# Kernel tuning notes

Hardware: AMD Instinct MI355X
Metric: run time of the kernel (lower is better)

The kernel has to match this reference:

```python
import jax, jax.numpy as jnp
import numpy as np

N, D = 8192, 256
NUM_CLASSES = 64


def setup_inputs() -> dict:
    key = jax.random.key(0)
    k1, k2 = jax.random.split(key)
    represent = jax.random.normal(k1, (N, D), dtype=jnp.float32)
    label = jax.random.randint(k2, (N,), 0, NUM_CLASSES, dtype=jnp.int64)
    t = jnp.float32(0.1)  # temperature
    return {"represent": represent, "label": label, "t": t}


def reference(represent, label, t):
    x = represent.astype(jnp.float32)                      # [N, D]
    norms = jnp.sqrt(jnp.sum(x * x, axis=-1))              # [N]
    # pairwise cosine: (x x^T) / (||xi|| ||xj||)
    cos = (x @ x.T) / (norms[:, None] * norms[None, :])    # [N, N]
    pos_mask = label[:, None] == label[None, :]            # [N, N] bool
    e = jnp.exp(cos / t)                                   # [N, N]
    # original computes exp(mask * cos / t): masked-out entries become exp(0) = 1
    pos_pair = jnp.where(pos_mask, e, 1.0).sum(axis=-1)    # [N]
    neg_pair = jnp.where(pos_mask, 1.0, e).sum(axis=-1)    # [N]
    loss = (jnp.log(neg_pair) - jnp.log(pos_pair)).sum() / represent.shape[0]
    return loss
```

## Files before the change

kernel.cpp:

```cpp
#include <hip/hip_runtime.h>
#include <hip/hip_bf16.h>

#define N_ROWS 8192
#define DIM 256
#define NUM_CLASSES 64
#define NBLK 64
#define NTRI (NBLK * (NBLK + 1) / 2)

typedef __bf16 bf16x8 __attribute__((ext_vector_type(8)));
typedef float f32x4 __attribute__((ext_vector_type(4)));

__device__ __forceinline__ unsigned short f2bf(float f) {
  unsigned int u = __float_as_uint(f);
  u += 0x7fffu + ((u >> 16) & 1u);
  return (unsigned short)(u >> 16);
}
__device__ __forceinline__ float bf2f(unsigned short h) {
  return __uint_as_float(((unsigned int)h) << 16);
}

__device__ __forceinline__ void gload_lds16(const unsigned short* g, unsigned short* l) {
  __builtin_amdgcn_global_load_lds(
      (const __attribute__((address_space(1))) unsigned int*)g,
      (__attribute__((address_space(3))) unsigned int*)l, 16, 0, 0);
}

__global__ void __launch_bounds__(256) prep_kernel(
    const float* __restrict__ x, const float* __restrict__ tptr,
    unsigned short* __restrict__ xb, float* __restrict__ sv,
    float* __restrict__ gsum, unsigned int* __restrict__ gcnt) {
  if (blockIdx.x == 0 && threadIdx.x == 0) { *gsum = 0.f; *gcnt = 0u; }
  const int row = blockIdx.x * 4 + (threadIdx.x >> 6);
  const int lane = threadIdx.x & 63;
  const float4 v = *reinterpret_cast<const float4*>(x + (size_t)row * DIM + lane * 4);
  const unsigned short q0 = f2bf(v.x), q1 = f2bf(v.y), q2 = f2bf(v.z), q3 = f2bf(v.w);
  const float f0 = bf2f(q0), f1 = bf2f(q1), f2 = bf2f(q2), f3 = bf2f(q3);
  float ss = f0 * f0 + f1 * f1 + f2 * f2 + f3 * f3;
  ushort4 u4; u4.x = q0; u4.y = q1; u4.z = q2; u4.w = q3;
  *reinterpret_cast<ushort4*>(xb + (size_t)row * DIM + lane * 4) = u4;
  for (int m = 32; m; m >>= 1) ss += __shfl_xor(ss, m, 64);
  if (lane == 0) {
    const float C = 1.4426950408889634f / tptr[0];
    sv[row] = sqrtf(C / ss);
  }
}

__global__ void __launch_bounds__(256, 3) main_kernel(
    const unsigned short* __restrict__ xb, const float* __restrict__ sv,
    const int* __restrict__ lab, float* __restrict__ part) {
  const int q = blockIdx.x;
  int I = (int)((129.0f - sqrtf(16641.0f - 8.0f * (float)q)) * 0.5f);
  while (I * (129 - I) / 2 > q) --I;
  while ((I + 1) * (128 - I) / 2 <= q) ++I;
  const int J = I + (q - I * (129 - I) / 2);

  __shared__ alignas(16) unsigned short Alds[128 * 32];
  __shared__ alignas(16) unsigned short Blds[128 * 32];
  float* red = reinterpret_cast<float*>(Alds);
  float (*colred)[128][2] = reinterpret_cast<float (*)[128][2]>(Blds);

  const int tid = threadIdx.x;
  const int wave = tid >> 6;
  const int lane = tid & 63;
  const int quad = lane >> 4;
  const int lc = lane & 15;
  const int wrow = (wave >> 1) * 64;
  const int wcol = (wave & 1) * 64;
  const int rowBase = I * 128;
  const int colBase = J * 128;

  f32x4 acc[4][4];
  const f32x4 zero4 = {0.f, 0.f, 0.f, 0.f};
  for (int mi = 0; mi < 4; ++mi)
    for (int ni = 0; ni < 4; ++ni) acc[mi][ni] = zero4;

  const int srow = lane >> 2;
  const int sseg = (lane & 3) * 8;

  for (int kb = 0; kb < 8; ++kb) {
    const int k0 = kb * 32;
    const unsigned short* gA =
        xb + (size_t)(rowBase + wave * 32 + srow) * DIM + k0 + sseg;
    gload_lds16(gA, &Alds[(wave * 32) * 32]);
    gload_lds16(gA + 16 * DIM, &Alds[(wave * 32 + 16) * 32]);
    const unsigned short* gB =
        xb + (size_t)(colBase + wave * 32 + srow) * DIM + k0 + sseg;
    gload_lds16(gB, &Blds[(wave * 32) * 32]);
    gload_lds16(gB + 16 * DIM, &Blds[(wave * 32 + 16) * 32]);
    __syncthreads();
    bf16x8 afr[4], bfr[4];
    for (int mi = 0; mi < 4; ++mi)
      afr[mi] = *reinterpret_cast<const bf16x8*>(
          &Alds[(wrow + mi * 16 + lc) * 32 + quad * 8]);
    for (int ni = 0; ni < 4; ++ni)
      bfr[ni] = *reinterpret_cast<const bf16x8*>(
          &Blds[(wcol + ni * 16 + lc) * 32 + quad * 8]);
    for (int mi = 0; mi < 4; ++mi)
      for (int ni = 0; ni < 4; ++ni)
        acc[mi][ni] = __builtin_amdgcn_mfma_f32_16x16x32_bf16(
            afr[mi], bfr[ni], acc[mi][ni], 0, 0, 0);
    __syncthreads();
  }

  red[tid] = 0.f;
  __syncthreads();

  float scol[4];
  int labc[4];
  for (int ni = 0; ni < 4; ++ni) {
    const int c = colBase + wcol + ni * 16 + lc;
    scol[ni] = sv[c];
    labc[ni] = lab[c];
  }
  float ctot[4] = {0.f, 0.f, 0.f, 0.f};
  float csame[4] = {0.f, 0.f, 0.f, 0.f};

  for (int mi = 0; mi < 4; ++mi) {
    for (int r = 0; r < 4; ++r) {
      const int lr = wrow + mi * 16 + quad * 4 + r;
      const int grow = rowBase + lr;
      const float si = sv[grow];
      const int li = lab[grow];
      float st = 0.f, sm = 0.f;
      for (int ni = 0; ni < 4; ++ni) {
        const float e = exp2f(acc[mi][ni][r] * si * scol[ni]);
        const float em = (li == labc[ni]) ? e : 0.f;
        st += e;
        sm += em;
        ctot[ni] += e;
        csame[ni] += em;
      }
      for (int m = 8; m; m >>= 1) {
        st += __shfl_xor(st, m, 64);
        sm += __shfl_xor(sm, m, 64);
      }
      if (lc == 0) {
        atomicAdd(&red[lr], st);
        atomicAdd(&red[128 + lr], sm);
      }
    }
  }

  if (J > I) {
    for (int ni = 0; ni < 4; ++ni) {
      float t2 = ctot[ni] + __shfl_xor(ctot[ni], 16, 64);
      t2 += __shfl_xor(t2, 32, 64);
      float s2 = csame[ni] + __shfl_xor(csame[ni], 16, 64);
      s2 += __shfl_xor(s2, 32, 64);
      if (quad == 0) {
        colred[0][wcol + ni * 16 + lc][wave >> 1] = t2;
        colred[1][wcol + ni * 16 + lc][wave >> 1] = s2;
      }
    }
  }
  __syncthreads();
  if (tid < 128) {
    part[(size_t)J * N_ROWS + rowBase + tid] = red[tid];
    part[(size_t)(64 + J) * N_ROWS + rowBase + tid] = red[128 + tid];
    if (J > I) {
      part[(size_t)I * N_ROWS + colBase + tid] =
          colred[0][tid][0] + colred[0][tid][1];
      part[(size_t)(64 + I) * N_ROWS + colBase + tid] =
          colred[1][tid][0] + colred[1][tid][1];
    }
  }
}

__global__ void __launch_bounds__(256) row_loss_kernel(
    const float* __restrict__ part, const int* __restrict__ lab,
    float* __restrict__ gsum, unsigned int* __restrict__ gcnt,
    float* __restrict__ out) {
  __shared__ int h[NUM_CLASSES];
  if (threadIdx.x < NUM_CLASSES) h[threadIdx.x] = 0;
  __syncthreads();
  for (int i = threadIdx.x; i < N_ROWS; i += 256) atomicAdd(&h[lab[i]], 1);
  __syncthreads();

  const int row = blockIdx.x * 256 + threadIdx.x;
  float st = 0.f, sm = 0.f;
  for (int b = 0; b < 64; ++b) {
    st += part[(size_t)b * N_ROWS + row];
    sm += part[(size_t)(64 + b) * N_ROWS + row];
  }
  const int c = h[lab[row]];
  const float pos = sm + (float)(N_ROWS - c);
  const float neg = (st - sm) + (float)c;
  float term = logf(neg) - logf(pos);
  for (int m = 32; m; m >>= 1) term += __shfl_xor(term, m, 64);
  __shared__ float wsum[4];
  const int lane = threadIdx.x & 63;
  const int wave = threadIdx.x >> 6;
  if (lane == 0) wsum[wave] = term;
  __syncthreads();
  if (threadIdx.x == 0) {
    const float bs = wsum[0] + wsum[1] + wsum[2] + wsum[3];
    atomicAdd(gsum, bs);
    __threadfence();
    const unsigned int t = atomicAdd(gcnt, 1u);
    if (t == (unsigned int)(N_ROWS / 256 - 1)) {
      const float total = atomicAdd(gsum, 0.0f);
      out[0] = total * (1.0f / (float)N_ROWS);
    }
  }
}

extern "C" void kernel_launch(void* const* d_in, const int* in_sizes, int n_in,
                              void* d_out, int out_size, void* d_ws, size_t ws_size,
                              hipStream_t stream) {
  const float* x = (const float*)d_in[0];
  const int* lab = (const int*)d_in[1];
  const float* t = (const float*)d_in[2];
  float* out = (float*)d_out;

  char* ws = (char*)d_ws;
  unsigned short* xb = (unsigned short*)ws;
  float* sv = (float*)(ws + (4u << 20));
  float* part = (float*)(ws + (4u << 20) + (32u << 10));
  float* gsum = (float*)(ws + (8u << 20) + (32u << 10));
  unsigned int* gcnt = (unsigned int*)(ws + (8u << 20) + (32u << 10) + 8);

  prep_kernel<<<N_ROWS / 4, 256, 0, stream>>>(x, t, xb, sv, gsum, gcnt);
  main_kernel<<<NTRI, 256, 0, stream>>>(xb, sv, lab, part);
  row_loss_kernel<<<N_ROWS / 256, 256, 0, stream>>>(part, lab, gsum, gcnt, out);
}
```

Before: 118.7 us.

## Fuse prep, Gram tiles and loss into one persistent cooperative kernel

```diff
diff --git a/kernel.cpp b/kernel.cpp
--- a/kernel.cpp
+++ b/kernel.cpp
@@ -1,11 +1,15 @@
 #include <hip/hip_runtime.h>
 #include <hip/hip_bf16.h>
+#include <hip/hip_cooperative_groups.h>
+
+namespace cg = cooperative_groups;
 
 #define N_ROWS 8192
 #define DIM 256
 #define NUM_CLASSES 64
 #define NBLK 64
 #define NTRI (NBLK * (NBLK + 1) / 2)
+#define COOP_GRID 512
 
 typedef __bf16 bf16x8 __attribute__((ext_vector_type(8)));
 typedef float f32x4 __attribute__((ext_vector_type(4)));
@@ -23,6 +27,218 @@
   __builtin_amdgcn_global_load_lds(
       (const __attribute__((address_space(1))) unsigned int*)g,
       (__attribute__((address_space(3))) unsigned int*)l, 16, 0, 0);
+}
+
+__device__ __forceinline__ void tri_decode(int q, int& I, int& J) {
+  int i = (int)((129.0f - sqrtf(16641.0f - 8.0f * (float)q)) * 0.5f);
+  while (i * (129 - i) / 2 > q) --i;
+  while ((i + 1) * (128 - i) / 2 <= q) ++i;
+  I = i;
+  J = i + (q - i * (129 - i) / 2);
+}
+
+__global__ void __launch_bounds__(256, 3) fused_kernel(
+    const float* __restrict__ x, const int* __restrict__ lab,
+    const float* __restrict__ tptr, unsigned short* __restrict__ xb,
+    float* __restrict__ sv, int* __restrict__ hpart, float* __restrict__ part,
+    float* __restrict__ bsum, float* __restrict__ out) {
+  __shared__ alignas(16) unsigned short Alds[2][4096];
+  __shared__ alignas(16) unsigned short Blds[2][4096];
+
+  const int tid = threadIdx.x;
+  const int wave = tid >> 6;
+  const int lane = tid & 63;
+  const int quad = lane >> 4;
+  const int lc = lane & 15;
+  cg::grid_group grid = cg::this_grid();
+
+  {
+    const float C = 1.4426950408889634f / tptr[0];
+    for (int rq = blockIdx.x; rq < N_ROWS / 4; rq += gridDim.x) {
+      const int row = rq * 4 + wave;
+      const float4 v =
+          *reinterpret_cast<const float4*>(x + (size_t)row * DIM + lane * 4);
+      const unsigned short q0 = f2bf(v.x), q1 = f2bf(v.y), q2 = f2bf(v.z),
+                           q3 = f2bf(v.w);
+      const float f0 = bf2f(q0), f1 = bf2f(q1), f2 = bf2f(q2), f3 = bf2f(q3);
+      float ss = f0 * f0 + f1 * f1 + f2 * f2 + f3 * f3;
+      ushort4 u4; u4.x = q0; u4.y = q1; u4.z = q2; u4.w = q3;
+      *reinterpret_cast<ushort4*>(xb + (size_t)row * DIM + lane * 4) = u4;
+      for (int m = 32; m; m >>= 1) ss += __shfl_xor(ss, m, 64);
+      if (lane == 0) sv[row] = sqrtf(C / ss);
+    }
+    if (blockIdx.x < 32) {
+      int* h = reinterpret_cast<int*>(&Blds[0][0]);
+      if (tid < NUM_CLASSES) h[tid] = 0;
+      __syncthreads();
+      atomicAdd(&h[lab[blockIdx.x * 256 + tid]], 1);
+      __syncthreads();
+      if (tid < NUM_CLASSES) hpart[blockIdx.x * NUM_CLASSES + tid] = h[tid];
+    }
+  }
+  grid.sync();
+
+  {
+    const int wrow = (wave >> 1) * 64;
+    const int wcol = (wave & 1) * 64;
+    const int srow = lane >> 2;
+    const int sseg = (lane & 3) * 8;
+    float* red = reinterpret_cast<float*>(&Alds[1][0]);
+    float (*colred)[128][2] = reinterpret_cast<float (*)[128][2]>(&Blds[1][0]);
+
+#define STAGE(rb, cb, kb, b)                                                  \
+  {                                                                           \
+    const int k0 = (kb) * 32;                                                 \
+    const unsigned short* gA =                                                \
+        xb + (size_t)((rb) + wave * 32 + srow) * DIM + k0 + sseg;             \
+    gload_lds16(gA, &Alds[b][(wave * 32) * 32]);                              \
+    gload_lds16(gA + 16 * DIM, &Alds[b][(wave * 32 + 16) * 32]);              \
+    const unsigned short* gB =                                                \
+        xb + (size_t)((cb) + wave * 32 + srow) * DIM + k0 + sseg;             \
+    gload_lds16(gB, &Blds[b][(wave * 32) * 32]);                              \
+    gload_lds16(gB + 16 * DIM, &Blds[b][(wave * 32 + 16) * 32]);              \
+  }
+
+    int q = blockIdx.x;
+    int I, J;
+    tri_decode(q, I, J);
+    int rowBase = I * 128, colBase = J * 128;
+    STAGE(rowBase, colBase, 0, 0)
+
+    while (q < NTRI) {
+      const int qn = q + gridDim.x;
+      const bool hasNext = qn < NTRI;
+      int In = 0, Jn = 0, rowN = 0, colN = 0;
+      if (hasNext) { tri_decode(qn, In, Jn); rowN = In * 128; colN = Jn * 128; }
+
+      f32x4 acc[4][4];
+      const f32x4 zero4 = {0.f, 0.f, 0.f, 0.f};
+      for (int mi = 0; mi < 4; ++mi)
+        for (int ni = 0; ni < 4; ++ni) acc[mi][ni] = zero4;
+
+      for (int kb = 0; kb < 8; ++kb) {
+        __syncthreads();
+        if (kb < 7) STAGE(rowBase, colBase, kb + 1, (kb + 1) & 1)
+        else if (hasNext) STAGE(rowN, colN, 0, 0)
+        const unsigned short* Ab = &Alds[kb & 1][0];
+        const unsigned short* Bb = &Blds[kb & 1][0];
+        bf16x8 afr[4], bfr[4];
+        for (int mi = 0; mi < 4; ++mi)
+          afr[mi] = *reinterpret_cast<const bf16x8*>(
+              &Ab[(wrow + mi * 16 + lc) * 32 + quad * 8]);
+        for (int ni = 0; ni < 4; ++ni)
+          bfr[ni] = *reinterpret_cast<const bf16x8*>(
+              &Bb[(wcol + ni * 16 + lc) * 32 + quad * 8]);
+        for (int mi = 0; mi < 4; ++mi)
+          for (int ni = 0; ni < 4; ++ni)
+            acc[mi][ni] = __builtin_amdgcn_mfma_f32_16x16x32_bf16(
+                afr[mi], bfr[ni], acc[mi][ni], 0, 0, 0);
+      }
+      __syncthreads();
+
+      red[tid] = 0.f;
+      __syncthreads();
+
+      float scol[4];
+      int labc[4];
+      for (int ni = 0; ni < 4; ++ni) {
+        const int c = colBase + wcol + ni * 16 + lc;
+        scol[ni] = sv[c];
+        labc[ni] = lab[c];
+      }
+      float ctot[4] = {0.f, 0.f, 0.f, 0.f};
+      float csame[4] = {0.f, 0.f, 0.f, 0.f};
+
+      for (int mi = 0; mi < 4; ++mi) {
+        for (int r = 0; r < 4; ++r) {
+          const int lr = wrow + mi * 16 + quad * 4 + r;
+          const int grow = rowBase + lr;
+          const float si = sv[grow];
+          const int li = lab[grow];
+          float st = 0.f, sm = 0.f;
+          for (int ni = 0; ni < 4; ++ni) {
+            const float e = exp2f(acc[mi][ni][r] * si * scol[ni]);
+            const float em = (li == labc[ni]) ? e : 0.f;
+            st += e;
+            sm += em;
+            ctot[ni] += e;
+            csame[ni] += em;
+          }
+          for (int m = 8; m; m >>= 1) {
+            st += __shfl_xor(st, m, 64);
+            sm += __shfl_xor(sm, m, 64);
+          }
+          if (lc == 0) {
+            atomicAdd(&red[lr], st);
+            atomicAdd(&red[128 + lr], sm);
+          }
+        }
+      }
+
+      if (J > I) {
+        for (int ni = 0; ni < 4; ++ni) {
+          float t2 = ctot[ni] + __shfl_xor(ctot[ni], 16, 64);
+          t2 += __shfl_xor(t2, 32, 64);
+          float s2 = csame[ni] + __shfl_xor(csame[ni], 16, 64);
+          s2 += __shfl_xor(s2, 32, 64);
+          if (quad == 0) {
+            colred[0][wcol + ni * 16 + lc][wave >> 1] = t2;
+            colred[1][wcol + ni * 16 + lc][wave >> 1] = s2;
+          }
+        }
+      }
+      __syncthreads();
+      if (tid < 128) {
+        part[(size_t)J * N_ROWS + rowBase + tid] = red[tid];
+        part[(size_t)(64 + J) * N_ROWS + rowBase + tid] = red[128 + tid];
+        if (J > I) {
+          part[(size_t)I * N_ROWS + colBase + tid] =
+              colred[0][tid][0] + colred[0][tid][1];
+          part[(size_t)(64 + I) * N_ROWS + colBase + tid] =
+              colred[1][tid][0] + colred[1][tid][1];
+        }
+      }
+      q = qn; I = In; J = Jn; rowBase = rowN; colBase = colN;
+    }
+#undef STAGE
+  }
+  grid.sync();
+
+  if (blockIdx.x < 32) {
+    int* h = reinterpret_cast<int*>(&Alds[0][0]);
+    float* wsum = reinterpret_cast<float*>(&Blds[0][0]);
+    if (tid < NUM_CLASSES) {
+      int s = 0;
+      for (int k = 0; k < 32; ++k) s += hpart[k * NUM_CLASSES + tid];
+      h[tid] = s;
+    }
+    __syncthreads();
+    const int row = blockIdx.x * 256 + tid;
+    float st = 0.f, sm = 0.f;
+#pragma unroll 8
+    for (int b = 0; b < 64; ++b) {
+      st += part[(size_t)b * N_ROWS + row];
+      sm += part[(size_t)(64 + b) * N_ROWS + row];
+    }
+    const int c = h[lab[row]];
+    const float pos = sm + (float)(N_ROWS - c);
+    const float neg = (st - sm) + (float)c;
+    float term = logf(neg) - logf(pos);
+    for (int m = 32; m; m >>= 1) term += __shfl_xor(term, m, 64);
+    if (lane == 0) wsum[wave] = term;
+    __syncthreads();
+    if (tid == 0) {
+      bsum[blockIdx.x] = wsum[0] + wsum[1] + wsum[2] + wsum[3];
+      __threadfence();
+    }
+  }
+  grid.sync();
+
+  if (blockIdx.x == 0 && tid < 64) {
+    float v = (tid < 32) ? bsum[tid] : 0.f;
+    for (int m = 32; m; m >>= 1) v += __shfl_xor(v, m, 64);
+    if (tid == 0) out[0] = v * (1.0f / (float)N_ROWS);
+  }
 }
 
 __global__ void __launch_bounds__(256) prep_kernel(
@@ -39,20 +255,15 @@
   ushort4 u4; u4.x = q0; u4.y = q1; u4.z = q2; u4.w = q3;
   *reinterpret_cast<ushort4*>(xb + (size_t)row * DIM + lane * 4) = u4;
   for (int m = 32; m; m >>= 1) ss += __shfl_xor(ss, m, 64);
-  if (lane == 0) {
-    const float C = 1.4426950408889634f / tptr[0];
-    sv[row] = sqrtf(C / ss);
-  }
+  if (lane == 0) sv[row] = sqrtf(1.4426950408889634f / tptr[0] / ss);
 }
 
 __global__ void __launch_bounds__(256, 3) main_kernel(
     const unsigned short* __restrict__ xb, const float* __restrict__ sv,
     const int* __restrict__ lab, float* __restrict__ part) {
   const int q = blockIdx.x;
-  int I = (int)((129.0f - sqrtf(16641.0f - 8.0f * (float)q)) * 0.5f);
-  while (I * (129 - I) / 2 > q) --I;
-  while ((I + 1) * (128 - I) / 2 <= q) ++I;
-  const int J = I + (q - I * (129 - I) / 2);
+  int I, J;
+  tri_decode(q, I, J);
 
   __shared__ alignas(16) unsigned short Alds[128 * 32];
   __shared__ alignas(16) unsigned short Blds[128 * 32];
@@ -125,10 +336,7 @@
       for (int ni = 0; ni < 4; ++ni) {
         const float e = exp2f(acc[mi][ni][r] * si * scol[ni]);
         const float em = (li == labc[ni]) ? e : 0.f;
-        st += e;
-        sm += em;
-        ctot[ni] += e;
-        csame[ni] += em;
+        st += e; sm += em; ctot[ni] += e; csame[ni] += em;
       }
       for (int m = 8; m; m >>= 1) {
         st += __shfl_xor(st, m, 64);
@@ -216,10 +424,19 @@
   unsigned short* xb = (unsigned short*)ws;
   float* sv = (float*)(ws + (4u << 20));
   float* part = (float*)(ws + (4u << 20) + (32u << 10));
-  float* gsum = (float*)(ws + (8u << 20) + (32u << 10));
-  unsigned int* gcnt = (unsigned int*)(ws + (8u << 20) + (32u << 10) + 8);
-
-  prep_kernel<<<N_ROWS / 4, 256, 0, stream>>>(x, t, xb, sv, gsum, gcnt);
-  main_kernel<<<NTRI, 256, 0, stream>>>(xb, sv, lab, part);
-  row_loss_kernel<<<N_ROWS / 256, 256, 0, stream>>>(part, lab, gsum, gcnt, out);
-}
+  int* hpart = (int*)(ws + (8u << 20) + (32u << 10));
+  float* bsum = (float*)(ws + (8u << 20) + (40u << 10));
+  float* gsum = (float*)(ws + (8u << 20) + (41u << 10));
+  unsigned int* gcnt = (unsigned int*)(ws + (8u << 20) + (41u << 10) + 8);
+
+  void* args[] = {(void*)&x,  (void*)&lab,   (void*)&t,    (void*)&xb,
+                  (void*)&sv, (void*)&hpart, (void*)&part, (void*)&bsum,
+                  (void*)&out};
+  hipError_t err = hipLaunchCooperativeKernel(
+      (const void*)fused_kernel, dim3(COOP_GRID), dim3(256), args, 0, stream);
+  if (err != hipSuccess) {
+    prep_kernel<<<N_ROWS / 4, 256, 0, stream>>>(x, t, xb, sv, gsum, gcnt);
+    main_kernel<<<NTRI, 256, 0, stream>>>(xb, sv, lab, part);
+    row_loss_kernel<<<N_ROWS / 256, 256, 0, stream>>>(part, lab, gsum, gcnt, out);
+  }
+}
```

After: 296.7 us. 2.5x slower.
